# Kernel tuning notes

Hardware: AMD Instinct MI355X
Metric: run time of the kernel (lower is better)

The kernel has to match this reference:

```python
import jax, jax.numpy as jnp
import numpy as np

B, L, K, D = 1024, 128, 16, 512
NUM_FEATURES, NUM_LABELS, NUM_NEG = 100000, 131072, 2048
EPS = 0.1
C = 2.0 + EPS  # spherical kernel constant


def safe_log(x, eps=1e-08):
    return jnp.log(jnp.maximum(x, eps))


def safe_normalize(x, axis=-1, eps=0.0001):
    norm = jnp.linalg.norm(x, axis=axis, keepdims=True)
    return x / jnp.maximum(norm, eps)


def setup_inputs() -> dict:
    key = jax.random.key(0)
    k0, k1, k2, k3, k4 = jax.random.split(key, 5)
    indices = jax.random.randint(k0, (B, L), 0, NUM_FEATURES)
    mask = jnp.ones((B, L), jnp.float32)
    labels = jax.random.randint(k1, (B, K), 0, NUM_LABELS)
    label_mask = jnp.ones((B, K), jnp.float32)
    neg_indices = jax.random.randint(k2, (NUM_NEG,), 0, NUM_LABELS)
    embed_table = jax.random.normal(k3, (NUM_FEATURES, D), jnp.float32) * 0.02
    W_kernel = jax.random.normal(k4, (D, NUM_LABELS), jnp.float32) * 0.02  # nnx.Linear kernel (in, out)
    return {"indices": indices, "mask": mask, "labels": labels,
            "label_mask": label_mask, "neg_indices": neg_indices,
            "embed_table": embed_table, "W_kernel": W_kernel}


def reference(indices, mask, labels, label_mask, neg_indices, embed_table, W_kernel):
    # MeanEmbedding encoder
    embeds = embed_table[indices]                                  # [B, L, D]
    sum_embeds = jnp.sum(embeds * mask[:, :, None], axis=1)        # [B, D]
    enc = sum_embeds / jnp.maximum(jnp.sum(mask, axis=1, keepdims=True), 1.0)
    query = safe_normalize(enc, axis=-1)                           # [B, D]
    W = safe_normalize(W_kernel.T, axis=-1)                        # [NUM_LABELS, D]

    safe_labels = jnp.maximum(labels, 0)
    all_indices = jnp.concatenate([safe_labels.reshape(-1), neg_indices])  # [B*K + NN]
    W_subset = W[all_indices]                                      # [B*K+NN, D]

    # spherical Yat kernel: dot^2 / max(C - 2*dot, eps)
    dot = jnp.clip(query @ W_subset.T, -0.999, 0.999)              # [B, B*K+NN]
    scores = dot ** 2 / jnp.maximum(C - 2.0 * dot, EPS)

    idx_offsets = jnp.arange(B)[:, None] * K + jnp.arange(K)[None, :]
    pos_scores = jnp.take_along_axis(scores, idx_offsets, axis=1)  # [B, K]
    neg_scores = scores[:, B * K:]                                 # [B, NN]
    all_scores = jnp.concatenate([pos_scores, neg_scores], axis=1) + 1e-08
    log_Z = jax.scipy.special.logsumexp(safe_log(all_scores), axis=1)
    log_probs = safe_log(pos_scores + 1e-08) - log_Z[:, None]
    return -jnp.sum(log_probs * label_mask) / (jnp.sum(label_mask) + 1e-06)
```

## Files before the change

### kernel.cpp

```cpp
#include <hip/hip_runtime.h>
#include <hip/hip_bf16.h>

#define BDIM 1024
#define LDIM 128
#define KDIM 16
#define DDIM 512
#define NLAB 131072
#define NNEG 2048
#define NPOS (BDIM * KDIM)
#define NSUB (NPOS + NNEG)
#define EPSV 0.1f
#define CV 2.1f
#define NBUCK 512
#define GT_BLOCKS ((NSUB / 64) * (DDIM / 64))

typedef __attribute__((ext_vector_type(8))) short s8v;
typedef __attribute__((ext_vector_type(4))) float f4v;

static __device__ __forceinline__ unsigned short f2bf(float x) {
    union { float f; unsigned u; } v; v.f = x;
    unsigned r = v.u + 0x7FFF + ((v.u >> 16) & 1);
    return (unsigned short)(r >> 16);
}
static __device__ __forceinline__ float bf2f(unsigned short h) {
    return __uint_as_float((unsigned)h << 16);
}

__global__ __launch_bounds__(256) void init_kernel(int* __restrict__ cnt,
                                                   float* __restrict__ norms2,
                                                   float* __restrict__ Zrow,
                                                   float* __restrict__ accum,
                                                   int* __restrict__ ticket) {
    int j = blockIdx.x * 256 + threadIdx.x;
    if (j < NSUB) norms2[j] = 0.f;
    if (j < NBUCK) cnt[j] = 0;
    if (j < BDIM) Zrow[j] = 0.f;
    if (j < 2) accum[j] = 0.f;
    if (j == 0) *ticket = 0;
}

__global__ __launch_bounds__(256) void count_kernel(const int* __restrict__ labels,
                                                    const int* __restrict__ negs,
                                                    int* __restrict__ all_idx,
                                                    int* __restrict__ cnt) {
    int j = blockIdx.x * 256 + threadIdx.x;
    if (j >= NSUB) return;
    int v = (j < NPOS) ? max(labels[j], 0) : negs[j - NPOS];
    all_idx[j] = v;
    atomicAdd(&cnt[v >> 8], 1);
}

__global__ __launch_bounds__(256) void scan_kernel(const int* __restrict__ cnt,
                                                   int* __restrict__ offs) {
    int t = threadIdx.x;
    int a0 = cnt[2 * t], a1 = cnt[2 * t + 1];
    int chunk = a0 + a1;
    int ts = chunk;
    int lane = t & 63, wid = t >> 6;
    #pragma unroll
    for (int off = 1; off < 64; off <<= 1) {
        int v = __shfl_up(ts, off, 64);
        if (lane >= off) ts += v;
    }
    __shared__ int wsum[4];
    if (lane == 63) wsum[wid] = ts;
    __syncthreads();
    int woff = 0;
    for (int w = 0; w < wid; ++w) woff += wsum[w];
    int incl = woff + ts;
    int excl = incl - chunk;
    offs[2 * t]     = excl;
    offs[2 * t + 1] = excl + a0;
}

__global__ __launch_bounds__(256) void place_kernel(const int* __restrict__ all_idx,
                                                    int* __restrict__ offs,
                                                    int* __restrict__ srt_v,
                                                    int* __restrict__ rank) {
    int j = blockIdx.x * 256 + threadIdx.x;
    if (j >= NSUB) return;
    int v = all_idx[j];
    int r = atomicAdd(&offs[v >> 8], 1);
    srt_v[r] = v;
    rank[j] = r;
}

__global__ __launch_bounds__(256) void main1_kernel(const float* __restrict__ Wk,
                                                    const int* __restrict__ srt_v,
                                                    unsigned short* __restrict__ WT,
                                                    float* __restrict__ norms2,
                                                    const int* __restrict__ indices,
                                                    const float* __restrict__ mask,
                                                    const float* __restrict__ embed,
                                                    float* __restrict__ query,
                                                    unsigned short* __restrict__ qbf) {
    int t = threadIdx.x;
    if (blockIdx.x < GT_BLOCKS) {
        __shared__ unsigned short tile[64][66];
        __shared__ float psum[64];
        int bt = blockIdx.x;
        int rt = bt % (NSUB / 64);
        int dt = bt / (NSUB / 64);
        int r0 = rt * 64, d0 = dt * 64;
        int l = t & 63, w = t >> 6;
        if (t < 64) psum[t] = 0.f;
        __syncthreads();
        int v = srt_v[r0 + l];
        float local = 0.f;
        #pragma unroll
        for (int i = 0; i < 16; ++i) {
            int dl = w * 16 + i;
            float f = __builtin_nontemporal_load(&Wk[(size_t)(d0 + dl) * NLAB + v]);
            unsigned short h = f2bf(f);
            tile[l][dl] = h;
            float bf = bf2f(h);
            local += bf * bf;
        }
        atomicAdd(&psum[l], local);
        __syncthreads();
        #pragma unroll
        for (int i = 0; i < 16; ++i) {
            int rr = w * 16 + i;
            WT[(size_t)(r0 + rr) * DDIM + d0 + l] = tile[rr][l];
        }
        if (t < 64) atomicAdd(&norms2[r0 + t], psum[t]);
    } else {
        __shared__ int   sidx[LDIM];
        __shared__ float smask[LDIM];
        __shared__ float red[4];
        __shared__ float snorm;
        int b = blockIdx.x - GT_BLOCKS;
        if (t < LDIM) {
            sidx[t]  = indices[b * LDIM + t];
            smask[t] = mask[b * LDIM + t];
        }
        __syncthreads();
        float ax = 0.f, ay = 0.f, msum = 0.f;
        #pragma unroll 2
        for (int l = 0; l < LDIM; l += 4) {
            int   i0 = sidx[l],   i1 = sidx[l + 1],  i2 = sidx[l + 2],  i3 = sidx[l + 3];
            float m0 = smask[l],  m1 = smask[l + 1], m2 = smask[l + 2], m3 = smask[l + 3];
            float2 r0 = *(const float2*)&embed[(size_t)i0 * DDIM + t * 2];
            float2 r1 = *(const float2*)&embed[(size_t)i1 * DDIM + t * 2];
            float2 r2 = *(const float2*)&embed[(size_t)i2 * DDIM + t * 2];
            float2 r3 = *(const float2*)&embed[(size_t)i3 * DDIM + t * 2];
            msum += m0 + m1 + m2 + m3;
            ax += m0 * r0.x + m1 * r1.x + m2 * r2.x + m3 * r3.x;
            ay += m0 * r0.y + m1 * r1.y + m2 * r2.y + m3 * r3.y;
        }
        float denom = fmaxf(msum, 1.0f);
        ax /= denom; ay /= denom;
        float ss = ax * ax + ay * ay;
        #pragma unroll
        for (int off = 32; off > 0; off >>= 1) ss += __shfl_down(ss, off, 64);
        int wid = t >> 6, lane = t & 63;
        if (lane == 0) red[wid] = ss;
        __syncthreads();
        if (t == 0) snorm = sqrtf(red[0] + red[1] + red[2] + red[3]);
        __syncthreads();
        float inv = 1.f / fmaxf(snorm, 1e-4f);
        float2 o = { ax * inv, ay * inv };
        *(float2*)&query[(size_t)b * DDIM + t * 2] = o;
        ushort2 ob = { f2bf(o.x), f2bf(o.y) };
        *(ushort2*)&qbf[(size_t)b * DDIM + t * 2] = ob;
    }
}

static __device__ __forceinline__ float score_of(float acc, float nn) {
    float dot = acc / nn;
    dot = fminf(fmaxf(dot, -0.999f), 0.999f);
    return dot * dot / fmaxf(CV - 2.f * dot, EPSV);
}

__global__ __launch_bounds__(256) void main2_kernel(const unsigned short* __restrict__ qbf,
                                                    const float* __restrict__ query,
                                                    const unsigned short* __restrict__ WT,
                                                    const int* __restrict__ rank,
                                                    const float* __restrict__ norms2,
                                                    float* __restrict__ pos_scores,
                                                    float* __restrict__ Zrow) {
    int t = threadIdx.x;
    int w = t >> 6, l = t & 63;
    if (blockIdx.x < (BDIM / 64) * (NNEG / 64)) {
        __shared__ float rowsum[64];
        int bx = blockIdx.x;
        int mt = bx & 15, nt = bx >> 4;
        int wm = w >> 1, wn = w & 1;
        int lr = l & 15, lg = l >> 4;
        int m0 = mt * 64 + wm * 32;
        int n0 = nt * 64 + wn * 32;
        if (t < 64) rowsum[t] = 0.f;
        __syncthreads();

        int rB0 = rank[NPOS + n0 + lr];
        int rB1 = rank[NPOS + n0 + 16 + lr];
        const unsigned short* a0p = qbf + (size_t)(m0 + lr) * DDIM + lg * 8;
        const unsigned short* a1p = qbf + (size_t)(m0 + 16 + lr) * DDIM + lg * 8;
        const unsigned short* b0p = WT + (size_t)rB0 * DDIM + lg * 8;
        const unsigned short* b1p = WT + (size_t)rB1 * DDIM + lg * 8;

        f4v acc00 = {0.f, 0.f, 0.f, 0.f}, acc01 = acc00, acc10 = acc00, acc11 = acc00;
        #pragma unroll
        for (int k0 = 0; k0 < DDIM; k0 += 32) {
            s8v a0 = *(const s8v*)(a0p + k0);
            s8v a1 = *(const s8v*)(a1p + k0);
            s8v b0 = *(const s8v*)(b0p + k0);
            s8v b1 = *(const s8v*)(b1p + k0);
            acc00 = __builtin_amdgcn_mfma_f32_16x16x32_bf16(a0, b0, acc00, 0, 0, 0);
            acc01 = __builtin_amdgcn_mfma_f32_16x16x32_bf16(a0, b1, acc01, 0, 0, 0);
            acc10 = __builtin_amdgcn_mfma_f32_16x16x32_bf16(a1, b0, acc10, 0, 0, 0);
            acc11 = __builtin_amdgcn_mfma_f32_16x16x32_bf16(a1, b1, acc11, 0, 0, 0);
        }

        float nn0 = fmaxf(sqrtf(norms2[rB0]), 1e-4f);
        float nn1 = fmaxf(sqrtf(norms2[rB1]), 1e-4f);
        float s[8];
        #pragma unroll
        for (int i = 0; i < 4; ++i) {
            s[i]     = score_of(acc00[i], nn0) + score_of(acc01[i], nn1);
            s[4 + i] = score_of(acc10[i], nn0) + score_of(acc11[i], nn1);
        }
        #pragma unroll
        for (int i = 0; i < 8; ++i) {
            s[i] += __shfl_xor(s[i], 1, 64);
            s[i] += __shfl_xor(s[i], 2, 64);
            s[i] += __shfl_xor(s[i], 4, 64);
            s[i] += __shfl_xor(s[i], 8, 64);
        }
        if (lr == 0) {
            #pragma unroll
            for (int i = 0; i < 4; ++i) {
                atomicAdd(&rowsum[wm * 32 + lg * 4 + i], s[i]);
                atomicAdd(&rowsum[wm * 32 + 16 + lg * 4 + i], s[4 + i]);
            }
        }
        __syncthreads();
        if (t < 64) atomicAdd(&Zrow[mt * 64 + t], rowsum[t]);
    } else {
        int px = blockIdx.x - (BDIM / 64) * (NNEG / 64);
        int b = px * 4 + w;
        int j = b * KDIM + (l & 15);
        int r = rank[j];
        int g = l >> 4;
        const unsigned short* wrow = WT + (size_t)r * DDIM + g * 128;
        const float* qrow = query + (size_t)b * DDIM + g * 128;
        float acc = 0.f;
        #pragma unroll
        for (int kk = 0; kk < 128; kk += 8) {
            ushort4 w0 = *(const ushort4*)&wrow[kk];
            ushort4 w1 = *(const ushort4*)&wrow[kk + 4];
            float4 q0 = *(const float4*)&qrow[kk];
            float4 q1 = *(const float4*)&qrow[kk + 4];
            acc += bf2f(w0.x) * q0.x + bf2f(w0.y) * q0.y + bf2f(w0.z) * q0.z + bf2f(w0.w) * q0.w
                 + bf2f(w1.x) * q1.x + bf2f(w1.y) * q1.y + bf2f(w1.z) * q1.z + bf2f(w1.w) * q1.w;
        }
        acc += __shfl_xor(acc, 16, 64);
        acc += __shfl_xor(acc, 32, 64);
        if (l < 16) {
            float nrm = fmaxf(sqrtf(norms2[r]), 1e-4f);
            float dot = fminf(fmaxf(acc / nrm, -0.999f), 0.999f);
            float sc = dot * dot / fmaxf(CV - 2.f * dot, EPSV);
            pos_scores[j] = sc;
            float s = sc;
            s += __shfl_xor(s, 1, 64); s += __shfl_xor(s, 2, 64);
            s += __shfl_xor(s, 4, 64); s += __shfl_xor(s, 8, 64);
            if (l == 0) atomicAdd(&Zrow[b], s);
        }
    }
}

__global__ __launch_bounds__(256) void finalize_kernel(const float* __restrict__ pos_scores,
                                                       const float* __restrict__ label_mask,
                                                       const float* __restrict__ Zrow,
                                                       float* __restrict__ accum,
                                                       int* __restrict__ ticket,
                                                       float* __restrict__ out) {
    int j = blockIdx.x * 256 + threadIdx.x;
    int b = j >> 4;
    float lm = label_mask[j];
    float logZ = logf(Zrow[b] + (float)(KDIM + NNEG) * 1e-8f);
    float v = lm * (logf(pos_scores[j] + 1e-8f) - logZ);
    #pragma unroll
    for (int off = 32; off > 0; off >>= 1) {
        v  += __shfl_down(v, off, 64);
        lm += __shfl_down(lm, off, 64);
    }
    __shared__ float rv[4], rl[4];
    int wid = threadIdx.x >> 6, lane = threadIdx.x & 63;
    if (lane == 0) { rv[wid] = v; rl[wid] = lm; }
    __syncthreads();
    if (threadIdx.x == 0) {
        atomicAdd(&accum[0], rv[0] + rv[1] + rv[2] + rv[3]);
        atomicAdd(&accum[1], rl[0] + rl[1] + rl[2] + rl[3]);
        __threadfence();
        int old = atomicAdd(ticket, 1);
        if (old == (int)gridDim.x - 1) {
            float a = atomicAdd(&accum[0], 0.f);
            float m = atomicAdd(&accum[1], 0.f);
            out[0] = -a / (m + 1e-6f);
        }
    }
}

extern "C" void kernel_launch(void* const* d_in, const int* in_sizes, int n_in,
                              void* d_out, int out_size, void* d_ws, size_t ws_size,
                              hipStream_t stream) {
    const int*   indices    = (const int*)  d_in[0];
    const float* mask       = (const float*)d_in[1];
    const int*   labels     = (const int*)  d_in[2];
    const float* label_mask = (const float*)d_in[3];
    const int*   negs       = (const int*)  d_in[4];
    const float* embed      = (const float*)d_in[5];
    const float* Wk         = (const float*)d_in[6];
    float* out = (float*)d_out;

    unsigned short* WT  = (unsigned short*)d_ws;
    float* query      = (float*)(WT + (size_t)NSUB * DDIM);
    unsigned short* qbf = (unsigned short*)(query + (size_t)BDIM * DDIM);
    int*   all_idx    = (int*)(qbf + (size_t)BDIM * DDIM);
    int*   srt_v      = all_idx + NSUB;
    int*   rank       = srt_v + NSUB;
    float* norms2     = (float*)(rank + NSUB);
    float* pos_scores = norms2 + NSUB;
    float* Zrow       = pos_scores + NPOS;
    float* accum      = Zrow + BDIM;
    int*   ticket     = (int*)(accum + 2);
    int*   cnt        = ticket + 1;
    int*   offs       = cnt + NBUCK;

    init_kernel<<<NSUB / 256, 256, 0, stream>>>(cnt, norms2, Zrow, accum, ticket);
    count_kernel<<<NSUB / 256, 256, 0, stream>>>(labels, negs, all_idx, cnt);
    scan_kernel<<<1, 256, 0, stream>>>(cnt, offs);
    place_kernel<<<NSUB / 256, 256, 0, stream>>>(all_idx, offs, srt_v, rank);
    main1_kernel<<<GT_BLOCKS + BDIM, 256, 0, stream>>>(Wk, srt_v, WT, norms2,
                                                       indices, mask, embed, query, qbf);
    main2_kernel<<<(BDIM / 64) * (NNEG / 64) + NPOS / 64, 256, 0, stream>>>(
        qbf, query, WT, rank, norms2, pos_scores, Zrow);
    finalize_kernel<<<NPOS / 256, 256, 0, stream>>>(pos_scores, label_mask, Zrow,
                                                    accum, ticket, out);
}
```

Baseline: 152.1 us.

## Stream full W_kernel column buckets coalesced instead of strided per-label gather

The transposed W gather now has each block load a contiguous 256-label by 64-dim tile of W_kernel with vector loads into LDS. It then scatters only the labels that fall in that bucket, in sorted order, into the bf16 WT buffer, with a wave reduction for the row norms. This replaces 4-byte strided reads per label with fully coalesced streaming, at the cost of reading the whole weight matrix rather than only the needed columns. The query encoder blocks are moved first in the grid and share the LDS tile.

```diff
diff --git a/kernel.cpp b/kernel.cpp
--- a/kernel.cpp
+++ b/kernel.cpp
@@ -12,10 +12,11 @@
 #define EPSV 0.1f
 #define CV 2.1f
 #define NBUCK 512
-#define GT_BLOCKS ((NSUB / 64) * (DDIM / 64))
+#define GT_BLOCKS (NBUCK * 8)
 
 typedef __attribute__((ext_vector_type(8))) short s8v;
 typedef __attribute__((ext_vector_type(4))) float f4v;
+typedef __attribute__((ext_vector_type(4))) float fv4;
 
 static __device__ __forceinline__ unsigned short f2bf(float x) {
     union { float f; unsigned u; } v; v.f = x;
@@ -87,6 +88,8 @@
 
 __global__ __launch_bounds__(256) void main1_kernel(const float* __restrict__ Wk,
                                                     const int* __restrict__ srt_v,
+                                                    const int* __restrict__ offs_end,
+                                                    const int* __restrict__ cnt,
                                                     unsigned short* __restrict__ WT,
                                                     float* __restrict__ norms2,
                                                     const int* __restrict__ indices,
@@ -94,42 +97,16 @@
                                                     const float* __restrict__ embed,
                                                     float* __restrict__ query,
                                                     unsigned short* __restrict__ qbf) {
+    __shared__ __align__(16) unsigned short tile[256][65];
     int t = threadIdx.x;
-    if (blockIdx.x < GT_BLOCKS) {
-        __shared__ unsigned short tile[64][66];
-        __shared__ float psum[64];
-        int bt = blockIdx.x;
-        int rt = bt % (NSUB / 64);
-        int dt = bt / (NSUB / 64);
-        int r0 = rt * 64, d0 = dt * 64;
-        int l = t & 63, w = t >> 6;
-        if (t < 64) psum[t] = 0.f;
-        __syncthreads();
-        int v = srt_v[r0 + l];
-        float local = 0.f;
-        #pragma unroll
-        for (int i = 0; i < 16; ++i) {
-            int dl = w * 16 + i;
-            float f = __builtin_nontemporal_load(&Wk[(size_t)(d0 + dl) * NLAB + v]);
-            unsigned short h = f2bf(f);
-            tile[l][dl] = h;
-            float bf = bf2f(h);
-            local += bf * bf;
-        }
-        atomicAdd(&psum[l], local);
-        __syncthreads();
-        #pragma unroll
-        for (int i = 0; i < 16; ++i) {
-            int rr = w * 16 + i;
-            WT[(size_t)(r0 + rr) * DDIM + d0 + l] = tile[rr][l];
-        }
-        if (t < 64) atomicAdd(&norms2[r0 + t], psum[t]);
-    } else {
-        __shared__ int   sidx[LDIM];
-        __shared__ float smask[LDIM];
-        __shared__ float red[4];
-        __shared__ float snorm;
-        int b = blockIdx.x - GT_BLOCKS;
+    int w = t >> 6, l = t & 63;
+
+    if (blockIdx.x < BDIM) {
+        int*   sidx  = (int*)&tile[0][0];
+        float* smask = (float*)&tile[16][0];
+        float* red   = (float*)&tile[32][0];
+        float* snorm = (float*)&tile[33][0];
+        int b = blockIdx.x;
         if (t < LDIM) {
             sidx[t]  = indices[b * LDIM + t];
             smask[t] = mask[b * LDIM + t];
@@ -137,9 +114,9 @@
         __syncthreads();
         float ax = 0.f, ay = 0.f, msum = 0.f;
         #pragma unroll 2
-        for (int l = 0; l < LDIM; l += 4) {
-            int   i0 = sidx[l],   i1 = sidx[l + 1],  i2 = sidx[l + 2],  i3 = sidx[l + 3];
-            float m0 = smask[l],  m1 = smask[l + 1], m2 = smask[l + 2], m3 = smask[l + 3];
+        for (int ll = 0; ll < LDIM; ll += 4) {
+            int   i0 = sidx[ll],   i1 = sidx[ll + 1],  i2 = sidx[ll + 2],  i3 = sidx[ll + 3];
+            float m0 = smask[ll],  m1 = smask[ll + 1], m2 = smask[ll + 2], m3 = smask[ll + 3];
             float2 r0 = *(const float2*)&embed[(size_t)i0 * DDIM + t * 2];
             float2 r1 = *(const float2*)&embed[(size_t)i1 * DDIM + t * 2];
             float2 r2 = *(const float2*)&embed[(size_t)i2 * DDIM + t * 2];
@@ -153,16 +130,45 @@
         float ss = ax * ax + ay * ay;
         #pragma unroll
         for (int off = 32; off > 0; off >>= 1) ss += __shfl_down(ss, off, 64);
-        int wid = t >> 6, lane = t & 63;
-        if (lane == 0) red[wid] = ss;
-        __syncthreads();
-        if (t == 0) snorm = sqrtf(red[0] + red[1] + red[2] + red[3]);
-        __syncthreads();
-        float inv = 1.f / fmaxf(snorm, 1e-4f);
+        if (l == 0) red[w] = ss;
+        __syncthreads();
+        if (t == 0) snorm[0] = sqrtf(red[0] + red[1] + red[2] + red[3]);
+        __syncthreads();
+        float inv = 1.f / fmaxf(snorm[0], 1e-4f);
         float2 o = { ax * inv, ay * inv };
         *(float2*)&query[(size_t)b * DDIM + t * 2] = o;
         ushort2 ob = { f2bf(o.x), f2bf(o.y) };
         *(ushort2*)&qbf[(size_t)b * DDIM + t * 2] = ob;
+    } else {
+        int bt = blockIdx.x - BDIM;
+        int g  = bt >> 3;
+        int dt = bt & 7;
+        int d0 = dt * 64;
+        #pragma unroll
+        for (int i = 0; i < 16; ++i) {
+            int dl = w * 16 + i;
+            fv4 v = __builtin_nontemporal_load(
+                (const fv4*)&Wk[(size_t)(d0 + dl) * NLAB + g * 256 + l * 4]);
+            tile[l * 4 + 0][dl] = f2bf(v.x);
+            tile[l * 4 + 1][dl] = f2bf(v.y);
+            tile[l * 4 + 2][dl] = f2bf(v.z);
+            tile[l * 4 + 3][dl] = f2bf(v.w);
+        }
+        __syncthreads();
+        int rend = offs_end[g];
+        int rbeg = rend - cnt[g];
+        for (int r = rbeg + w; r < rend; r += 4) {
+            int v = srt_v[r];
+            int col = v - g * 256;
+            unsigned short h = tile[col][l];
+            WT[(size_t)r * DDIM + d0 + l] = h;
+            float f = bf2f(h);
+            float ss = f * f;
+            ss += __shfl_xor(ss, 1, 64);  ss += __shfl_xor(ss, 2, 64);
+            ss += __shfl_xor(ss, 4, 64);  ss += __shfl_xor(ss, 8, 64);
+            ss += __shfl_xor(ss, 16, 64); ss += __shfl_xor(ss, 32, 64);
+            if (l == 0) atomicAdd(&norms2[r], ss);
+        }
     }
 }
 
@@ -332,7 +338,7 @@
     count_kernel<<<NSUB / 256, 256, 0, stream>>>(labels, negs, all_idx, cnt);
     scan_kernel<<<1, 256, 0, stream>>>(cnt, offs);
     place_kernel<<<NSUB / 256, 256, 0, stream>>>(all_idx, offs, srt_v, rank);
-    main1_kernel<<<GT_BLOCKS + BDIM, 256, 0, stream>>>(Wk, srt_v, WT, norms2,
+    main1_kernel<<<BDIM + GT_BLOCKS, 256, 0, stream>>>(Wk, srt_v, offs, cnt, WT, norms2,
                                                        indices, mask, embed, query, qbf);
     main2_kernel<<<(BDIM / 64) * (NNEG / 64) + NPOS / 64, 256, 0, stream>>>(
         qbf, query, WT, rank, norms2, pos_scores, Zrow);
```

New measurement: 148.7 us. 2.3% less time.
